# Performance work log

Hardware: AMD Instinct MI355X
Metric: run time of the kernel (lower is better)

Reference implementation:

```python
import jax, jax.numpy as jnp
import numpy as np
from math import sqrt

B, T, E, W, H = 4, 512, 1024, 64, 16
DK = E // H


def _make_position_mask(T, W):
    # mask[s, w, t] = 1 iff token s is the w-th neighbor in the window around t
    t = np.arange(T)[None, :]            # [1, T]
    w = np.arange(W)[:, None]            # [W, 1]
    idx = np.clip(t - W // 2 + w, 0, T - 1)  # [W, T] source index per (w, t)
    mask = np.zeros((T, W, T), dtype=np.float32)
    mask[idx, np.arange(W)[:, None], np.arange(T)[None, :]] = 1.0
    return jnp.asarray(mask)


def setup_inputs() -> dict:
    key = jax.random.key(0)
    ks = jax.random.split(key, 7)
    s = 1.0 / sqrt(E)
    return {
        "x": jax.random.normal(ks[0], (B, T, E), jnp.float32),
        "position_mask": _make_position_mask(T, W),
        "Wq": jax.random.normal(ks[1], (E, E), jnp.float32) * s,
        "bq": jnp.zeros((E,), jnp.float32),
        "Wv": jax.random.normal(ks[2], (E, E), jnp.float32) * s,
        "bv": jnp.zeros((E,), jnp.float32),
        "Wo": jax.random.normal(ks[3], (E, E), jnp.float32) * s,
        "bo": jnp.zeros((E,), jnp.float32),
    }


def reference(x, position_mask, Wq, bq, Wv, bv, Wo, bo):
    # gather window neighbors: attend_inputs[b,t,w,e] = sum_s x[b,s,e] * mask[s,w,t]
    attend = jnp.einsum('bse,swt->btwe', x, position_mask)  # [B,T,W,E]

    # NOTE: original splits E as (d_k, H) with d_k-major (view(..., d_k, H))
    q = (x @ Wq + bq).reshape(B, T, DK, H)                    # [B,T,DK,H]
    q = q.transpose(0, 3, 1, 2)                               # [B,H,T,DK]
    k = (attend @ Wq + bq).reshape(B, T, W, DK, H)            # key uses query_transform (as in source)
    k = k.transpose(0, 4, 1, 2, 3)                            # [B,H,T,W,DK]
    v = (attend @ Wv + bv).reshape(B, T, W, DK, H)
    v = v.transpose(0, 4, 1, 2, 3)                            # [B,H,T,W,DK]

    scores = jnp.einsum('bhtd,bhtwd->bhtw', q, k) / sqrt(E)   # scale by sqrt(E), as in source
    probs = jax.nn.softmax(scores, axis=-1)                   # softmax over window W
    out = jnp.einsum('bhtw,bhtwd->bhtd', probs, v)            # [B,H,T,DK]
    out = out.transpose(0, 2, 1, 3).reshape(B, T, E)          # merge (H, DK) H-major, as in source reshape
    return out @ Wo + bo
```

## Files before the change

### kernel.cpp

```cpp
#include <hip/hip_runtime.h>
#include <hip/hip_bf16.h>

typedef __attribute__((ext_vector_type(8))) short short8;
typedef __attribute__((ext_vector_type(4))) float f32x4;

constexpr int NB = 4, NT = 512, NE = 1024, NH = 16;
constexpr int NBT = 2048;
constexpr int TT = 32;

__device__ inline short f2bf(float f) {
    __hip_bfloat16 h = __float2bfloat16(f);
    return __builtin_bit_cast(short, h);
}

__global__ __launch_bounds__(256) void transpose_w_kernel(const float* __restrict__ W0,
                                                          const float* __restrict__ W1,
                                                          const float* __restrict__ W2,
                                                          short* __restrict__ WTall) {
    const float* W = blockIdx.z == 0 ? W0 : (blockIdx.z == 1 ? W1 : W2);
    const bool perm = blockIdx.z < 2;
    short* WT = WTall + (size_t)blockIdx.z * NE * NE;

    __shared__ float tile[64][65];
    const int e0 = blockIdx.y * 64, j0 = blockIdx.x * 64;
    const int el = threadIdx.x & 63, grp = threadIdx.x >> 6;
    for (int i = grp; i < 64; i += 4)
        tile[i][el] = W[(size_t)(e0 + i) * NE + j0 + el];
    __syncthreads();
    for (int it = grp; it < 64; it += 4) {
        int j = j0 + it;
        int jp = perm ? ((j & 15) * 64 + (j >> 4)) : j;
        WT[(size_t)jp * NE + e0 + el] = f2bf(tile[el][it]);
    }
}

template <int BM, int BN, int THREADS, int LOG_GX, bool A_F32, bool ZT_DUAL, bool PERM_BIAS, bool OUT_BF16>
__global__ __launch_bounds__(THREADS) void mfma_gemm_kernel(const void* __restrict__ Xv,
                                                            const short* __restrict__ WT,
                                                            const float* __restrict__ bias0,
                                                            const float* __restrict__ bias1,
                                                            void* __restrict__ out0,
                                                            short* __restrict__ outZt) {
    constexpr int WAVES = THREADS / 64;
    constexpr int WAVE_M = BM / (WAVES / 2), WAVE_N = BN / 2;
    constexpr int MR = WAVE_M / 16, NR = WAVE_N / 16;
    constexpr int RDA = BM * 8 / THREADS, RDB = BN * 8 / THREADS;

    __shared__ short As[BM * 64];
    __shared__ short Bs[BN * 64];
    const int tid = threadIdx.x;
    const int lane = tid & 63, wid = tid >> 6;

    const int nwg = (1 << LOG_GX) * gridDim.y;
    const int bid = blockIdx.y * (1 << LOG_GX) + blockIdx.x;
    const int swz = (bid & 7) * (nwg >> 3) + (bid >> 3);
    const int r0 = (swz >> LOG_GX) * BM;
    const int c0 = (swz & ((1 << LOG_GX) - 1)) * BN;
    const int wr = (wid >> 1) * WAVE_M, wc = (wid & 1) * WAVE_N;
    const bool isZ = ZT_DUAL && (c0 >= NE);

    f32x4 acc[MR][NR];
#pragma unroll
    for (int m = 0; m < MR; m++)
#pragma unroll
        for (int n = 0; n < NR; n++) acc[m][n] = (f32x4){0.f, 0.f, 0.f, 0.f};

    short8 pfA[RDA], pfB[RDB];
    auto load_tiles = [&](int k0) {
#pragma unroll
        for (int rd = 0; rd < RDA; rd++) {
            int slot = rd * (THREADS * 16) + tid * 16;
            int row  = slot >> 7;
            int c    = ((slot >> 4) & 7) ^ (row & 7);
            if (A_F32) {
                const float* xa = (const float*)Xv + (size_t)(r0 + row) * NE + k0 + c * 8;
                float4 a = *(const float4*)xa, b = *(const float4*)(xa + 4);
                short8 v;
                v[0] = f2bf(a.x); v[1] = f2bf(a.y); v[2] = f2bf(a.z); v[3] = f2bf(a.w);
                v[4] = f2bf(b.x); v[5] = f2bf(b.y); v[6] = f2bf(b.z); v[7] = f2bf(b.w);
                pfA[rd] = v;
            } else {
                pfA[rd] = *(const short8*)((const short*)Xv + (size_t)(r0 + row) * NE + k0 + c * 8);
            }
        }
#pragma unroll
        for (int rd = 0; rd < RDB; rd++) {
            int slot = rd * (THREADS * 16) + tid * 16;
            int row  = slot >> 7;
            int c    = ((slot >> 4) & 7) ^ (row & 7);
            pfB[rd] = *(const short8*)(WT + (size_t)(c0 + row) * NE + k0 + c * 8);
        }
    };

    load_tiles(0);
    for (int k0 = 0; k0 < NE; k0 += 64) {
        __syncthreads();
#pragma unroll
        for (int rd = 0; rd < RDA; rd++)
            *(short8*)((char*)As + rd * (THREADS * 16) + tid * 16) = pfA[rd];
#pragma unroll
        for (int rd = 0; rd < RDB; rd++)
            *(short8*)((char*)Bs + rd * (THREADS * 16) + tid * 16) = pfB[rd];
        __syncthreads();
        if (k0 + 64 < NE) load_tiles(k0 + 64);

#pragma unroll
        for (int kk = 0; kk < 2; kk++) {
            short8 af[MR], bf[NR];
            const int cidx = kk * 4 + (lane >> 4);
#pragma unroll
            for (int m = 0; m < MR; m++) {
                int row = wr + m * 16 + (lane & 15);
                af[m] = *(const short8*)((char*)As + row * 128 + ((cidx ^ (row & 7)) * 16));
            }
#pragma unroll
            for (int n = 0; n < NR; n++) {
                int row = wc + n * 16 + (lane & 15);
                bf[n] = *(const short8*)((char*)Bs + row * 128 + ((cidx ^ (row & 7)) * 16));
            }
            if (isZ) {
#pragma unroll
                for (int m = 0; m < MR; m++)
#pragma unroll
                    for (int n = 0; n < NR; n++)
                        acc[m][n] = __builtin_amdgcn_mfma_f32_16x16x32_bf16(bf[n], af[m], acc[m][n], 0, 0, 0);
            } else {
#pragma unroll
                for (int m = 0; m < MR; m++)
#pragma unroll
                    for (int n = 0; n < NR; n++)
                        acc[m][n] = __builtin_amdgcn_mfma_f32_16x16x32_bf16(af[m], bf[n], acc[m][n], 0, 0, 0);
            }
        }
    }

    if (isZ) {
        const int cb = c0 - NE;
        const int tok = r0 + wr + (lane & 15);
#pragma unroll
        for (int m = 0; m < MR; m++)
#pragma unroll
            for (int n = 0; n < NR; n++)
#pragma unroll
                for (int r = 0; r < 4; r++) {
                    int jp = cb + wc + n * 16 + (lane >> 4) * 4 + r;
                    float bb = bias1[(jp & 63) * 16 + (jp >> 6)];
                    outZt[(size_t)jp * NBT + tok + m * 16] = f2bf(acc[m][n][r] + bb);
                }
    } else {
        short* outS = (short*)out0;
        float* outF = (float*)out0;
#pragma unroll
        for (int m = 0; m < MR; m++)
#pragma unroll
            for (int n = 0; n < NR; n++) {
                int lc   = c0 + wc + n * 16 + (lane & 15);
                int bsrc = PERM_BIAS ? ((lc & 63) * 16 + (lc >> 6)) : lc;
                float bb = bias0[bsrc];
#pragma unroll
                for (int r = 0; r < 4; r++) {
                    int row = r0 + wr + m * 16 + (lane >> 4) * 4 + r;
                    float val = acc[m][n][r] + bb;
                    if (OUT_BF16) outS[(size_t)row * NE + lc] = f2bf(val);
                    else          outF[(size_t)row * NE + lc] = val;
                }
            }
    }
}

__global__ __launch_bounds__(256) void attn_kernel(const short* __restrict__ Yb,
                                                   const short* __restrict__ Zt,
                                                   short* __restrict__ Mb) {
    __shared__ __align__(16) short KS[96][64];
    __shared__ __align__(16) short VT[64][96];
    __shared__ __align__(16) float SL[32][100];
    __shared__ __align__(16) short PL[32][104];
    __shared__ float RED[32][17];

    const int t0 = blockIdx.x * TT;
    const int h  = blockIdx.y;
    const int b  = blockIdx.z;
    const int tid = threadIdx.x;
    const int lane = tid & 63, wid = tid >> 6;

    for (int u = tid; u < 416; u += 256)
        *(short8*)((short*)PL + u * 8) = (short8){0, 0, 0, 0, 0, 0, 0, 0};

    for (int u = tid; u < 768; u += 256) {
        int r = u >> 3, c = u & 7;
        int ts = t0 - 32 + r;
        ts = ts < 0 ? 0 : (ts > NT - 1 ? NT - 1 : ts);
        short8 kv = *(const short8*)(Yb + ((size_t)b * NT + ts) * NE + h * 64 + c * 8);
        *(short8*)&KS[r][(c ^ (r & 7)) * 8] = kv;
    }
    {
        const int d = tid >> 2, cbase = (tid & 3) * 3;
        const short* zr = Zt + (size_t)(h * 64 + d) * NBT + b * NT;
#pragma unroll
        for (int i = 0; i < 3; i++) {
            int ch = cbase + i;
            int s0 = t0 - 32 + ch * 8;
            short8 v;
            if (s0 >= 0 && s0 <= NT - 8) {
                v = *(const short8*)(zr + s0);
            } else {
#pragma unroll
                for (int j = 0; j < 8; j++) {
                    int ss = s0 + j;
                    ss = ss < 0 ? 0 : (ss > NT - 1 ? NT - 1 : ss);
                    v[j] = zr[ss];
                }
            }
            *(short8*)&VT[d][ch * 8] = v;
        }
    }
    __syncthreads();

    {
        const int mq = wid >> 1, ntrio = (wid & 1) * 3;
        f32x4 sacc[3];
#pragma unroll
        for (int ni = 0; ni < 3; ni++) sacc[ni] = (f32x4){0.f, 0.f, 0.f, 0.f};
#pragma unroll
        for (int ks = 0; ks < 2; ks++) {
            const int cidx = ks * 4 + (lane >> 4);
            int qrow = 32 + mq * 16 + (lane & 15);
            short8 af = *(const short8*)((char*)KS + qrow * 128 + ((cidx ^ (qrow & 7)) * 16));
#pragma unroll
            for (int ni = 0; ni < 3; ni++) {
                int srow = (ntrio + ni) * 16 + (lane & 15);
                short8 bf = *(const short8*)((char*)KS + srow * 128 + ((cidx ^ (srow & 7)) * 16));
                sacc[ni] = __builtin_amdgcn_mfma_f32_16x16x32_bf16(af, bf, sacc[ni], 0, 0, 0);
            }
        }
#pragma unroll
        for (int ni = 0; ni < 3; ni++)
#pragma unroll
            for (int r = 0; r < 4; r++)
                SL[mq * 16 + (lane >> 4) * 4 + r][(ntrio + ni) * 16 + (lane & 15)] =
                    sacc[ni][r] * 0.03125f;
    }
    __syncthreads();

    {
        const int tl = tid & (TT - 1), oct = tid >> 5;
        float sv[8];
#pragma unroll
        for (int wi = 0; wi < 8; wi++) sv[wi] = SL[tl][tl + oct * 8 + wi];
        float lmax = sv[0];
#pragma unroll
        for (int wi = 1; wi < 8; wi++) lmax = fmaxf(lmax, sv[wi]);
        RED[tl][oct] = lmax;
        __syncthreads();
        float gmax = RED[tl][0];
#pragma unroll
        for (int i = 1; i < 8; i++) gmax = fmaxf(gmax, RED[tl][i]);
        float lsum = 0.f;
#pragma unroll
        for (int wi = 0; wi < 8; wi++) {
            float e = __expf(sv[wi] - gmax);
            PL[tl][tl + oct * 8 + wi] = f2bf(e);
            lsum += e;
        }
        RED[tl][8 + oct] = lsum;
        __syncthreads();
        float gsum = RED[tl][8];
#pragma unroll
        for (int i = 9; i < 16; i++) gsum += RED[tl][i];
        if (oct == 0) RED[tl][16] = 1.0f / gsum;
    }
    __syncthreads();

    {
        const int mp = wid >> 1, npair = (wid & 1) * 2;
        f32x4 oacc[2];
#pragma unroll
        for (int ni = 0; ni < 2; ni++) oacc[ni] = (f32x4){0.f, 0.f, 0.f, 0.f};
#pragma unroll
        for (int ks = 0; ks < 3; ks++) {
            int prow = mp * 16 + (lane & 15);
            short8 pa = *(const short8*)((char*)PL + prow * 208 + ks * 64 + (lane >> 4) * 16);
#pragma unroll
            for (int ni = 0; ni < 2; ni++) {
                int d = (npair + ni) * 16 + (lane & 15);
                short8 bv = *(const short8*)((char*)VT + d * 192 + ks * 64 + (lane >> 4) * 16);
                oacc[ni] = __builtin_amdgcn_mfma_f32_16x16x32_bf16(pa, bv, oacc[ni], 0, 0, 0);
            }
        }
#pragma unroll
        for (int ni = 0; ni < 2; ni++) {
            int d = (npair + ni) * 16 + (lane & 15);
#pragma unroll
            for (int r = 0; r < 4; r++) {
                int tl = mp * 16 + (lane >> 4) * 4 + r;
                float inv = RED[tl][16];
                Mb[((size_t)b * NT + t0 + tl) * NE + h * 64 + d] = f2bf(oacc[ni][r] * inv);
            }
        }
    }
}

extern "C" void kernel_launch(void* const* d_in, const int* in_sizes, int n_in,
                              void* d_out, int out_size, void* d_ws, size_t ws_size,
                              hipStream_t stream) {
    const float* x  = (const float*)d_in[0];
    const float* Wq = (const float*)d_in[2];
    const float* bq = (const float*)d_in[3];
    const float* Wv = (const float*)d_in[4];
    const float* bv = (const float*)d_in[5];
    const float* Wo = (const float*)d_in[6];
    const float* bo = (const float*)d_in[7];
    float* outp = (float*)d_out;

    char* wsb = (char*)d_ws;
    short* WTa = (short*)(wsb);
    short* Yb  = (short*)(wsb + (6u << 20));
    short* Zt  = (short*)(wsb + (10u << 20));
    short* Mb  = (short*)(wsb + (14u << 20));
    short* WTo = WTa + 2 * (size_t)NE * NE;

    transpose_w_kernel<<<dim3(16, 16, 3), 256, 0, stream>>>(Wq, Wv, Wo, WTa);

    mfma_gemm_kernel<128, 128, 512, 4, true, true, true, true>
        <<<dim3(2 * NE / 128, NBT / 128), 512, 0, stream>>>(x, WTa, bq, bv, Yb, Zt);

    attn_kernel<<<dim3(NT / TT, NH, NB), 256, 0, stream>>>(Yb, Zt, Mb);

    mfma_gemm_kernel<64, 128, 256, 3, false, false, false, false>
        <<<dim3(NE / 128, NBT / 64), 256, 0, stream>>>(Mb, WTo, bo, nullptr, (void*)outp, nullptr);
}
```

Measured before the change: 173.6 us.

## Double-buffer GEMM tiles via direct global-to-LDS loads and pre-convert x to bf16

The GEMM kernel now stages A and B tiles straight into LDS with global_load_lds, keeping two LDS buffers so the next k-tile loads while the current one is multiplied. This removes the register round-trip and one of the two barriers per iteration. The fp32-to-bf16 conversion of x moves out of the first GEMM's inner loop into an extended prep kernel that writes a bf16 copy, so both GEMMs read bf16 A. The cost is doubled LDS per block, which may reduce occupancy, and an extra pass over x.

```diff
diff --git a/kernel.cpp b/kernel.cpp
--- a/kernel.cpp
+++ b/kernel.cpp
@@ -13,10 +13,30 @@
     return __builtin_bit_cast(short, h);
 }
 
-__global__ __launch_bounds__(256) void transpose_w_kernel(const float* __restrict__ W0,
-                                                          const float* __restrict__ W1,
-                                                          const float* __restrict__ W2,
-                                                          short* __restrict__ WTall) {
+#define GLOAD16(g, l) \
+    __builtin_amdgcn_global_load_lds((const __attribute__((address_space(1))) void*)(g), \
+                                     (__attribute__((address_space(3))) void*)(l), 16, 0, 0)
+
+__global__ __launch_bounds__(256) void prep_kernel(const float* __restrict__ x,
+                                                   const float* __restrict__ W0,
+                                                   const float* __restrict__ W1,
+                                                   const float* __restrict__ W2,
+                                                   short* __restrict__ WTall,
+                                                   short* __restrict__ Xb) {
+    if (blockIdx.z == 3) {
+        const int gid = blockIdx.y * 16 + blockIdx.x;
+        size_t base = (size_t)gid * 8192 + threadIdx.x * 8;
+#pragma unroll
+        for (int it = 0; it < 4; it++) {
+            const float4* p = (const float4*)(x + base + it * 2048);
+            float4 a = p[0], b = p[1];
+            short8 v;
+            v[0] = f2bf(a.x); v[1] = f2bf(a.y); v[2] = f2bf(a.z); v[3] = f2bf(a.w);
+            v[4] = f2bf(b.x); v[5] = f2bf(b.y); v[6] = f2bf(b.z); v[7] = f2bf(b.w);
+            *(short8*)(Xb + base + it * 2048) = v;
+        }
+        return;
+    }
     const float* W = blockIdx.z == 0 ? W0 : (blockIdx.z == 1 ? W1 : W2);
     const bool perm = blockIdx.z < 2;
     short* WT = WTall + (size_t)blockIdx.z * NE * NE;
@@ -34,8 +54,8 @@
     }
 }
 
-template <int BM, int BN, int THREADS, int LOG_GX, bool A_F32, bool ZT_DUAL, bool PERM_BIAS, bool OUT_BF16>
-__global__ __launch_bounds__(THREADS) void mfma_gemm_kernel(const void* __restrict__ Xv,
+template <int BM, int BN, int THREADS, int LOG_GX, bool ZT_DUAL, bool PERM_BIAS, bool OUT_BF16>
+__global__ __launch_bounds__(THREADS) void mfma_gemm_kernel(const short* __restrict__ A,
                                                             const short* __restrict__ WT,
                                                             const float* __restrict__ bias0,
                                                             const float* __restrict__ bias1,
@@ -44,10 +64,11 @@
     constexpr int WAVES = THREADS / 64;
     constexpr int WAVE_M = BM / (WAVES / 2), WAVE_N = BN / 2;
     constexpr int MR = WAVE_M / 16, NR = WAVE_N / 16;
-    constexpr int RDA = BM * 8 / THREADS, RDB = BN * 8 / THREADS;
-
-    __shared__ short As[BM * 64];
-    __shared__ short Bs[BN * 64];
+    constexpr int ASZ = BM * 64, BSZ = BN * 64;
+    constexpr int SWA = BM * 128 / (THREADS * 16);
+    constexpr int SWB = BN * 128 / (THREADS * 16);
+
+    __shared__ __align__(16) short LB[2][ASZ + BSZ];
     const int tid = threadIdx.x;
     const int lane = tid & 63, wid = tid >> 6;
 
@@ -65,45 +86,35 @@
 #pragma unroll
         for (int n = 0; n < NR; n++) acc[m][n] = (f32x4){0.f, 0.f, 0.f, 0.f};
 
-    short8 pfA[RDA], pfB[RDB];
-    auto load_tiles = [&](int k0) {
-#pragma unroll
-        for (int rd = 0; rd < RDA; rd++) {
-            int slot = rd * (THREADS * 16) + tid * 16;
-            int row  = slot >> 7;
-            int c    = ((slot >> 4) & 7) ^ (row & 7);
-            if (A_F32) {
-                const float* xa = (const float*)Xv + (size_t)(r0 + row) * NE + k0 + c * 8;
-                float4 a = *(const float4*)xa, b = *(const float4*)(xa + 4);
-                short8 v;
-                v[0] = f2bf(a.x); v[1] = f2bf(a.y); v[2] = f2bf(a.z); v[3] = f2bf(a.w);
-                v[4] = f2bf(b.x); v[5] = f2bf(b.y); v[6] = f2bf(b.z); v[7] = f2bf(b.w);
-                pfA[rd] = v;
-            } else {
-                pfA[rd] = *(const short8*)((const short*)Xv + (size_t)(r0 + row) * NE + k0 + c * 8);
-            }
-        }
-#pragma unroll
-        for (int rd = 0; rd < RDB; rd++) {
-            int slot = rd * (THREADS * 16) + tid * 16;
-            int row  = slot >> 7;
-            int c    = ((slot >> 4) & 7) ^ (row & 7);
-            pfB[rd] = *(const short8*)(WT + (size_t)(c0 + row) * NE + k0 + c * 8);
+    auto stage = [&](int buf, int k0) {
+        char* Ab = (char*)&LB[buf][0];
+        char* Bb = (char*)&LB[buf][ASZ];
+#pragma unroll
+        for (int s = 0; s < SWA; s++) {
+            int wb  = s * (THREADS * 16) + wid * 1024;
+            int off = wb + lane * 16;
+            int row = off >> 7;
+            int c   = ((off >> 4) & 7) ^ (row & 7);
+            GLOAD16(A + (size_t)(r0 + row) * NE + k0 + c * 8, Ab + wb);
+        }
+#pragma unroll
+        for (int s = 0; s < SWB; s++) {
+            int wb  = s * (THREADS * 16) + wid * 1024;
+            int off = wb + lane * 16;
+            int row = off >> 7;
+            int c   = ((off >> 4) & 7) ^ (row & 7);
+            GLOAD16(WT + (size_t)(c0 + row) * NE + k0 + c * 8, Bb + wb);
         }
     };
 
-    load_tiles(0);
+    stage(0, 0);
+    __syncthreads();
+
+    int cur = 0;
     for (int k0 = 0; k0 < NE; k0 += 64) {
-        __syncthreads();
-#pragma unroll
-        for (int rd = 0; rd < RDA; rd++)
-            *(short8*)((char*)As + rd * (THREADS * 16) + tid * 16) = pfA[rd];
-#pragma unroll
-        for (int rd = 0; rd < RDB; rd++)
-            *(short8*)((char*)Bs + rd * (THREADS * 16) + tid * 16) = pfB[rd];
-        __syncthreads();
-        if (k0 + 64 < NE) load_tiles(k0 + 64);
-
+        if (k0 + 64 < NE) stage(cur ^ 1, k0 + 64);
+        const char* Ab = (const char*)&LB[cur][0];
+        const char* Bb = (const char*)&LB[cur][ASZ];
 #pragma unroll
         for (int kk = 0; kk < 2; kk++) {
             short8 af[MR], bf[NR];
@@ -111,12 +122,12 @@
 #pragma unroll
             for (int m = 0; m < MR; m++) {
                 int row = wr + m * 16 + (lane & 15);
-                af[m] = *(const short8*)((char*)As + row * 128 + ((cidx ^ (row & 7)) * 16));
+                af[m] = *(const short8*)(Ab + row * 128 + ((cidx ^ (row & 7)) * 16));
             }
 #pragma unroll
             for (int n = 0; n < NR; n++) {
                 int row = wc + n * 16 + (lane & 15);
-                bf[n] = *(const short8*)((char*)Bs + row * 128 + ((cidx ^ (row & 7)) * 16));
+                bf[n] = *(const short8*)(Bb + row * 128 + ((cidx ^ (row & 7)) * 16));
             }
             if (isZ) {
 #pragma unroll
@@ -132,6 +143,8 @@
                         acc[m][n] = __builtin_amdgcn_mfma_f32_16x16x32_bf16(af[m], bf[n], acc[m][n], 0, 0, 0);
             }
         }
+        __syncthreads();
+        cur ^= 1;
     }
 
     if (isZ) {
@@ -314,18 +327,19 @@
 
     char* wsb = (char*)d_ws;
     short* WTa = (short*)(wsb);
-    short* Yb  = (short*)(wsb + (6u << 20));
-    short* Zt  = (short*)(wsb + (10u << 20));
-    short* Mb  = (short*)(wsb + (14u << 20));
+    short* Xb  = (short*)(wsb + (6u << 20));
+    short* Yb  = (short*)(wsb + (10u << 20));
+    short* Zt  = (short*)(wsb + (14u << 20));
+    short* Mb  = (short*)(wsb + (18u << 20));
     short* WTo = WTa + 2 * (size_t)NE * NE;
 
-    transpose_w_kernel<<<dim3(16, 16, 3), 256, 0, stream>>>(Wq, Wv, Wo, WTa);
-
-    mfma_gemm_kernel<128, 128, 512, 4, true, true, true, true>
-        <<<dim3(2 * NE / 128, NBT / 128), 512, 0, stream>>>(x, WTa, bq, bv, Yb, Zt);
+    prep_kernel<<<dim3(16, 16, 4), 256, 0, stream>>>(x, Wq, Wv, Wo, WTa, Xb);
+
+    mfma_gemm_kernel<128, 128, 512, 4, true, true, true>
+        <<<dim3(2 * NE / 128, NBT / 128), 512, 0, stream>>>(Xb, WTa, bq, bv, Yb, Zt);
 
     attn_kernel<<<dim3(NT / TT, NH, NB), 256, 0, stream>>>(Yb, Zt, Mb);
 
-    mfma_gemm_kernel<64, 128, 256, 3, false, false, false, false>
+    mfma_gemm_kernel<64, 128, 256, 3, false, false, false>
         <<<dim3(NE / 128, NBT / 64), 256, 0, stream>>>(Mb, WTo, bo, nullptr, (void*)outp, nullptr);
 }
```

New measurement: 156.5 us. -9.8%, faster.
